# Kernel tuning notes

Hardware: AMD Instinct MI355X
Metric: run time of the kernel (lower is better)

The kernel has to match this reference:

```python
import math
import jax, jax.numpy as jnp
import numpy as np

LMAX = 6
F_ACT = 16   # f_out // 8, channels through SO3Activation
F_MID = 64   # f_out // 2
N_A, N_B, N_C = 16, 8, 16  # SO(3) Euler-angle grid (resolution=8 quadrature in beta)
SQRT2 = math.sqrt(2.0)     # normalize2mom factor for relu

# ---- Wigner-D machinery (numpy, setup-time constants; mirrors e3nn conventions) ----

def _su2_generators(j):
    m = np.arange(-j, j)
    raising = np.diag(-np.sqrt(j * (j + 1) - m * (m + 1)), k=-1).astype(complex)
    m = np.arange(-j + 1, j + 1)
    lowering = np.diag(np.sqrt(j * (j + 1) - m * (m - 1)), k=1).astype(complex)
    m = np.arange(-j, j + 1)
    return np.stack([0.5 * (raising + lowering), np.diag(1j * m), -0.5j * (raising - lowering)])

def _q_real(l):
    q = np.zeros((2 * l + 1, 2 * l + 1), dtype=complex)
    for m in range(-l, 0):
        q[l + m, l + abs(m)] = 2 ** -0.5
        q[l + m, l - abs(m)] = -1j * 2 ** -0.5
    q[l, l] = 1
    for m in range(1, l + 1):
        q[l + m, l + abs(m)] = (-1) ** m * 2 ** -0.5
        q[l + m, l - abs(m)] = 1j * (-1) ** m * 2 ** -0.5
    return (-1j) ** l * q

def _so3_generators(l):
    X = _su2_generators(l)
    Q = _q_real(l)
    return np.real(np.einsum('ij,njk,kl->nil', np.conj(Q.T), X, Q))

def _expm(A):
    w, V = np.linalg.eig(A.astype(complex))
    return np.real((V * np.exp(w)) @ np.linalg.inv(V))

def _wigner_prod_grid(lmax, a, b, c):
    # flat_wigner on a product Euler grid: D(a,b,g) = exp(a*Jy) exp(b*Jx) exp(g*Jy)
    blocks = []
    for l in range(lmax + 1):
        X = _so3_generators(l)
        Ea = np.stack([_expm(t * X[1]) for t in a])
        Eb = np.stack([_expm(t * X[0]) for t in b])
        Ec = np.stack([_expm(t * X[1]) for t in c])
        D = np.einsum('amn,bnp,cpq->abcmq', Ea, Eb, Ec)
        blocks.append((2 * l + 1) ** 0.5 * D.reshape(len(a) * len(b) * len(c), -1))
    return np.concatenate(blocks, -1)

def _flat_wigner_pts(lmax, a, b, c):
    blocks = []
    for l in range(lmax + 1):
        X = _so3_generators(l)
        D = np.stack([_expm(ai * X[1]) @ _expm(bi * X[0]) @ _expm(ci * X[1]) for ai, bi, ci in zip(a, b, c)])
        blocks.append((2 * l + 1) ** 0.5 * D.reshape(len(a), -1))
    return np.concatenate(blocks, -1)

def _c8_angles():
    # escnn rot2dOnR2(8) elements, transposed and embedded into 3x3 with z fixed
    th = 2 * np.pi * np.arange(8) / 8
    M = np.zeros((8, 3, 3))
    M[:, 0, 0] = np.cos(th); M[:, 0, 1] = np.sin(th)
    M[:, 1, 0] = -np.sin(th); M[:, 1, 1] = np.cos(th)
    M[:, 2, 2] = 1.0
    x = M @ np.array([0.0, 1.0, 0.0])
    b = np.arccos(np.clip(x[:, 1], -1, 1))
    a = np.arctan2(x[:, 0], x[:, 2])
    def my(t): c, s = np.cos(t), np.sin(t); return np.array([[c, 0, s], [0, 1, 0], [-s, 0, c]])
    def mx(t): c, s = np.cos(t), np.sin(t); return np.array([[1, 0, 0], [0, c, -s], [0, s, c]])
    g = np.array([np.arctan2(R[0, 2], R[0, 0]) for R in [(my(a[i]) @ mx(b[i])).T @ M[i] for i in range(8)]])
    return a, b, g

# ---- precomputed constants ----
_A = 2 * np.pi * np.arange(N_A) / N_A
_XB, _WB = np.polynomial.legendre.leggauss(N_B)
_B = np.arccos(_XB)
_C = 2 * np.pi * np.arange(N_C) / N_C
D_IN = jnp.asarray(_wigner_prod_grid(1, _A, _B, _C), jnp.float32)                 # (G, 10)
_QW = np.broadcast_to((_WB / 2.0)[None, :, None] / (N_A * N_C), (N_A, N_B, N_C)).reshape(-1)
D_OUTW = jnp.asarray(_wigner_prod_grid(LMAX, _A, _B, _C) * _QW[:, None], jnp.float32)  # (G, 455), quadrature folded in
C8W = jnp.asarray(_flat_wigner_pts(LMAX, *_c8_angles()), jnp.float32)             # (8, 455)


def setup_inputs() -> dict:
    key = jax.random.key(0)
    ks = jax.random.split(key, 16)
    inp = {
        'x': jax.random.normal(ks[0], (16, 32, 128, 455), jnp.float32),
        'trajectory': jax.random.normal(ks[1], (16, 32, 10), jnp.float32),
        'w1_l0': jax.random.normal(ks[2], (1, F_ACT, 1, 1), jnp.float32),
        'w1_l1': jax.random.normal(ks[3], (1, F_ACT, 3, 3), jnp.float32),
    }
    for l in range(LMAX + 1):
        d = 2 * l + 1
        inp[f'w2_l{l}'] = jax.random.normal(ks[4 + l], (F_ACT, F_MID, d, d), jnp.float32)
    return inp


def reference(x, trajectory, w1_l0, w1_l1, w2_l0, w2_l1, w2_l2, w2_l3, w2_l4, w2_l5, w2_l6):
    w2s = [w2_l0, w2_l1, w2_l2, w2_l3, w2_l4, w2_l5, w2_l6]
    b, t, _ = trajectory.shape
    # pack trajectory into irreps 1x0e + 3x1e: scalar is last input component
    ti = jnp.concatenate([trajectory[..., 9:10], trajectory[..., :9]], axis=-1)  # (b,t,10)
    # proj_1 (o3.Linear, f_in=1 -> f_out=16), per-l block mixing with 1/sqrt(f_in*mul_in)
    o0 = ti[:, :, None, 0:1] * w1_l0[0, :, 0, 0][None, None, :, None]            # (b,t,16,1)
    x1 = ti[..., 1:10].reshape(b, t, 3, 3)                                       # (mul=3, m=3)
    o1 = jnp.einsum('btum,guw->btgwm', x1, w1_l1[0]) * (3.0 ** -0.5)             # (b,t,16,3,3)
    feat = jnp.concatenate([o0, o1.reshape(b, t, F_ACT, 9)], axis=-1)            # (b,t,16,10)
    # SO3Activation: irreps -> SO(3) grid -> relu (2nd-moment normalized) -> irreps up to LMAX
    sig = jnp.einsum('btci,gi->btcg', feat, D_IN)                                # (b,t,16,G)
    sig = jax.nn.relu(sig) * SQRT2
    feat = jnp.einsum('btcg,gi->btci', sig, D_OUTW)                              # (b,t,16,455)
    # proj_2 (o3.Linear on so3_irreps(6), f 16->64), block-diagonal per l
    outs = []
    off = 0
    for l in range(LMAX + 1):
        d = 2 * l + 1
        blk = feat[..., off:off + d * d].reshape(b, t, F_ACT, d, d)
        o = jnp.einsum('btfum,fguw->btgwm', blk, w2s[l]) * ((F_ACT * d) ** -0.5)
        outs.append(o.reshape(b, t, F_MID, d * d))
        off += d * d
    traj_out = jnp.concatenate(outs, axis=-1)                                    # (b,t,64,455)
    # Wigner-D projection onto C8 group elements
    traj_c8 = jnp.einsum('btcj,ij->btci', traj_out, C8W)                         # (b,t,64,8)
    x_c8 = jnp.einsum('bhcj,ij->bhci', x, C8W)                                   # (b,h,128,8)
    return x_c8, traj_c8
```

## Files before the change

### kernel.cpp

```cpp
#include <hip/hip_runtime.h>
#include <hip/hip_bf16.h>
#include <math.h>


typedef __attribute__((ext_vector_type(8))) short bf16x8;
typedef __attribute__((ext_vector_type(4))) float f32x4;
typedef __attribute__((ext_vector_type(16))) float f32x16;

__device__ const int c_offs[8] = {0, 1, 10, 35, 84, 165, 286, 455};

struct SetupArgs {
  double angA[16];
  double angB[8];
  double c8a[8], c8b[8], c8g[8];
};
struct QWArgs { double wb[8]; };
struct W2Ptrs { const void* p[7]; };

__device__ __forceinline__ float bf2f(unsigned short u) {
  union { unsigned int i; float f; } v; v.i = ((unsigned int)u) << 16; return v.f;
}
__device__ __forceinline__ unsigned short f2bf(float f) {
  union { float f; unsigned int i; } v; v.f = f;
  unsigned int r = v.i + 0x7fffu + ((v.i >> 16) & 1u);
  return (unsigned short)(r >> 16);
}
__device__ __forceinline__ float in_val(const void* p, size_t i, int isf) {
  return isf ? ((const float*)p)[i] : bf2f(((const unsigned short*)p)[i]);
}
__device__ __forceinline__ void gl_lds16(const void* g, void* lds) {
  __builtin_amdgcn_global_load_lds(
      (const __attribute__((address_space(1))) unsigned int*)g,
      (__attribute__((address_space(3))) unsigned int*)lds, 16, 0, 0);
}

__global__ __launch_bounds__(192) void k_exps(SetupArgs args, double* exps,
                                              const void* x, int* flag) {
  __shared__ double Qr[169], Qi[169], Bm[169], R[169];
  __shared__ double coefA[13], coefB[13], rowsum[13];
  __shared__ double snorm;
  __shared__ int cnt;
  int tid = threadIdx.x;

  if (blockIdx.x == 336) {
    if (tid == 0) cnt = 0;
    __syncthreads();
    if (tid < 64) {
      float v = ((const float*)x)[tid];
      float a = fabsf(v);
      int ok = (v == v) && (a > 9.0949470e-13f) && (a < 1.0995116e12f);
      atomicAdd(&cnt, ok);
    }
    __syncthreads();
    if (tid == 0) *flag = (cnt >= 32) ? 1 : 0;
    return;
  }

  int l = blockIdx.x / 48, item = blockIdx.x % 48;
  int e = tid;
  bool val = (e < 169);
  int r = e / 13, c = e % 13;

  if (val) { Qr[e] = 0.0; Qi[e] = 0.0; }
  __syncthreads();
  if (tid == 0) {
    const double is2 = 0.70710678118654752440;
    for (int m = -l; m <= l; m++) {
      int rr = l + m;
      if (m < 0) {
        Qr[rr * 13 + (l - m)] = is2;
        Qi[rr * 13 + (l + m)] = -is2;
      } else if (m == 0) {
        Qr[l * 13 + l] = 1.0;
      } else {
        double s = (m & 1) ? -1.0 : 1.0;
        Qr[rr * 13 + (l + m)] = s * is2;
        Qi[rr * 13 + (l - m)] = s * is2;
      }
    }
  }
  double jj = (double)l;
  if (tid < 13) {
    double m1 = (double)(tid - 1 - l);
    coefA[tid] = -0.5 * sqrt(fmax(jj * (jj + 1.0) - m1 * (m1 + 1.0), 0.0));
    double m2 = (double)(tid + 1 - l);
    coefB[tid] = 0.5 * sqrt(fmax(jj * (jj + 1.0) - m2 * (m2 - 1.0), 0.0));
  }
  __syncthreads();
  {
    int lm = l & 3;
    double pr = (lm == 0) ? 1.0 : (lm == 2 ? -1.0 : 0.0);
    double pi = (lm == 1) ? -1.0 : (lm == 3 ? 1.0 : 0.0);
    if (val) {
      double qr = Qr[e], qi = Qi[e];
      Qr[e] = qr * pr - qi * pi;
      Qi[e] = qr * pi + qi * pr;
    }
  }
  __syncthreads();

  double t; int axis;
  if (item < 16)      { t = args.angA[item];      axis = 1; }
  else if (item < 24) { t = args.angB[item - 16]; axis = 0; }
  else if (item < 32) { t = args.c8a[item - 24];  axis = 1; }
  else if (item < 40) { t = args.c8b[item - 32];  axis = 0; }
  else                { t = args.c8g[item - 40];  axis = 1; }

  if (val) {
    double accr = 0.0;
    if (axis == 1) {
#pragma unroll
      for (int p = 0; p < 13; p++) {
        double mp = (double)(p - l);
        double ar = Qr[p * 13 + r], ai = -Qi[p * 13 + r];
        double br = Qr[p * 13 + c], bi = Qi[p * 13 + c];
        accr += -mp * (ar * bi + ai * br);
      }
    } else {
#pragma unroll
      for (int p = 0; p < 13; p++) {
        double xr = 0.0, xi = 0.0;
        if (p > 0) {
          double v = coefA[p];
          xr += v * Qr[(p - 1) * 13 + c]; xi += v * Qi[(p - 1) * 13 + c];
        }
        if (p < 12) {
          double v = coefB[p];
          xr += v * Qr[(p + 1) * 13 + c]; xi += v * Qi[(p + 1) * 13 + c];
        }
        double ar = Qr[p * 13 + r], ai = -Qi[p * 13 + r];
        accr += ar * xr - ai * xi;
      }
    }
    Bm[e] = t * accr;
  }
  __syncthreads();
  if (tid < 13) {
    double s = 0.0;
#pragma unroll
    for (int cc = 0; cc < 13; cc++) s += fabs(Bm[tid * 13 + cc]);
    rowsum[tid] = s;
  }
  __syncthreads();
  if (tid == 0) {
    double mx = 0.0;
#pragma unroll
    for (int rr = 0; rr < 13; rr++) mx = fmax(mx, rowsum[rr]);
    int s = 0;
    while (mx > 0.5 && s < 48) { mx *= 0.5; s++; }
    snorm = (double)s;
  }
  __syncthreads();
  int sq = (int)snorm;
  double sc = 1.0;
  for (int i = 0; i < sq; i++) sc *= 0.5;
  if (val) {
    double b = Bm[e] * sc;
    Bm[e] = b;
    R[e] = b / 16.0 + ((r == c) ? 1.0 : 0.0);
  }
  __syncthreads();
  for (int k = 15; k >= 1; k--) {
    double acc = 0.0;
    if (val) {
#pragma unroll
      for (int p = 0; p < 13; p++) acc += Bm[r * 13 + p] * R[p * 13 + c];
    }
    __syncthreads();
    if (val) R[e] = acc / (double)k + ((r == c) ? 1.0 : 0.0);
    __syncthreads();
  }
  for (int i = 0; i < sq; i++) {
    double acc = 0.0;
    if (val) {
#pragma unroll
      for (int p = 0; p < 13; p++) acc += R[r * 13 + p] * R[p * 13 + c];
    }
    __syncthreads();
    if (val) R[e] = acc;
    __syncthreads();
  }
  double* out = exps + (size_t)blockIdx.x * 169;
  if (val) out[e] = R[e];
}

__global__ __launch_bounds__(192) void k_assemble(const double* exps, QWArgs qw,
                                                  unsigned short* dwt, float* dint,
                                                  float* c8w,
                                                  const void* traj, const void* w1l0,
                                                  const void* w1l1, float* feat,
                                                  const int* flag) {
  __shared__ double Ea[169], Eb[169], Ec[169], T1[169];
  int tid = threadIdx.x;
  int bx = blockIdx.x;

  if (bx >= 952) {
    int isf = __builtin_amdgcn_readfirstlane(flag[0]);
    int idx = (bx - 952) * 192 + tid;
    if (idx >= 512 * 160) return;
    int bt = idx / 160, rem = idx % 160;
    int c = rem / 10, i = rem % 10;
    float v;
    if (i == 0) {
      v = in_val(traj, bt * 10 + 9, isf) * in_val(w1l0, c, isf);
    } else {
      int ii = i - 1, w = ii / 3, m = ii % 3;
      float acc = 0.0f;
      for (int u = 0; u < 3; u++)
        acc += in_val(traj, bt * 10 + 3 * u + m, isf) *
               in_val(w1l1, c * 9 + u * 3 + w, isf);
      v = acc * 0.57735026918962576f;
    }
    feat[idx] = v;
    return;
  }

  int e = tid;
  bool valp = (e < 169);
  int r = e / 13, c = e % 13;

  if (bx >= 896) {
    int idx = bx - 896;
    int l = idx / 8, ci = idx % 8;
    int d = 2 * l + 1;
    const double* pa = exps + (size_t)(l * 48 + 24 + ci) * 169;
    const double* pb = exps + (size_t)(l * 48 + 32 + ci) * 169;
    const double* pc = exps + (size_t)(l * 48 + 40 + ci) * 169;
    if (valp) { Ea[e] = pa[e]; Eb[e] = pb[e]; Ec[e] = pc[e]; }
    __syncthreads();
    if (valp) {
      double acc = 0.0;
#pragma unroll
      for (int p = 0; p < 13; p++) acc += Ea[r * 13 + p] * Eb[p * 13 + c];
      T1[e] = acc;
    }
    __syncthreads();
    double scale = sqrt((double)(2 * l + 1));
    if (valp) {
      double acc = 0.0;
#pragma unroll
      for (int p = 0; p < 13; p++) acc += T1[r * 13 + p] * Ec[p * 13 + c];
      if (r < d && c < d)
        c8w[ci * 512 + c_offs[l] + r * d + c] = (float)(scale * acc);
    }
    if (l == 0) {
      for (int jz = 455 + tid; jz < 512; jz += 192)
        c8w[ci * 512 + jz] = 0.0f;
    }
    return;
  }

  int l = bx >> 7, rem = bx & 127;
  int a = rem >> 3, b = rem & 7;
  int d = 2 * l + 1;
  const double* pa = exps + (size_t)(l * 48 + a) * 169;
  const double* pb = exps + (size_t)(l * 48 + 16 + b) * 169;
  if (valp) { Ea[e] = pa[e]; Eb[e] = pb[e]; }
  __syncthreads();
  if (valp) {
    double acc = 0.0;
#pragma unroll
    for (int p = 0; p < 13; p++) acc += Ea[r * 13 + p] * Eb[p * 13 + c];
    T1[e] = acc;
  }
  double scale = sqrt((double)(2 * l + 1));
  double qwv = qw.wb[b] * (1.0 / 512.0);
  bool inblk = valp && (r < d) && (c < d);
  int j = inblk ? (c_offs[l] + r * d + c) : 0;
  int g0 = a * 128 + b * 16;
  const double* ctab = exps + (size_t)(l * 48) * 169;
  unsigned int ow[8];
  float dv[16];
#pragma unroll
  for (int cc = 0; cc < 16; cc++) {
    __syncthreads();
    if (valp) Ec[e] = ctab[(size_t)cc * 169 + e];
    __syncthreads();
    double acc = 0.0;
    if (valp) {
#pragma unroll
      for (int p = 0; p < 13; p++) acc += T1[r * 13 + p] * Ec[p * 13 + c];
    }
    unsigned int hv = (unsigned int)f2bf((float)(scale * acc * qwv));
    if ((cc & 1) == 0) ow[cc >> 1] = hv;
    else               ow[cc >> 1] |= hv << 16;
    dv[cc] = (float)(scale * acc);
  }
  if (inblk) {
    unsigned short* wp = &dwt[(size_t)j * 2048 + g0];
    *(uint4*)&wp[0] = make_uint4(ow[0], ow[1], ow[2], ow[3]);
    *(uint4*)&wp[8] = make_uint4(ow[4], ow[5], ow[6], ow[7]);
    if (l == 1) {
      float* dp = &dint[(size_t)(1 + r * 3 + c) * 2048 + g0];
      *(float4*)&dp[0]  = make_float4(dv[0],  dv[1],  dv[2],  dv[3]);
      *(float4*)&dp[4]  = make_float4(dv[4],  dv[5],  dv[6],  dv[7]);
      *(float4*)&dp[8]  = make_float4(dv[8],  dv[9],  dv[10], dv[11]);
      *(float4*)&dp[12] = make_float4(dv[12], dv[13], dv[14], dv[15]);
    }
    if (l == 0) {
      float* dp = &dint[g0];
      *(float4*)&dp[0]  = make_float4(dv[0],  dv[1],  dv[2],  dv[3]);
      *(float4*)&dp[4]  = make_float4(dv[4],  dv[5],  dv[6],  dv[7]);
      *(float4*)&dp[8]  = make_float4(dv[8],  dv[9],  dv[10], dv[11]);
      *(float4*)&dp[12] = make_float4(dv[12], dv[13], dv[14], dv[15]);
    }
  }
  if (l == 0 && tid < 57) {
    unsigned short* zp = &dwt[(size_t)(455 + tid) * 2048 + g0];
    *(uint4*)&zp[0] = make_uint4(0, 0, 0, 0);
    *(uint4*)&zp[8] = make_uint4(0, 0, 0, 0);
  }
}

__global__ __launch_bounds__(256) void k_post(const float* feat, const float* dint,
                                              unsigned short* sig, W2Ptrs w2,
                                              const float* c8w, unsigned short* et,
                                              const int* flag) {
  int bx = blockIdx.x;
  if (bx < 4096) {
    int bi = bx >> 3;
    int g = ((bx & 7) << 8) + threadIdx.x;
    float din[10];
#pragma unroll
    for (int i = 0; i < 10; i++) din[i] = dint[(size_t)i * 2048 + g];
    const float* fr = feat + bi * 160;
    for (int cc = 0; cc < 16; cc++) {
      float acc = 0.0f;
#pragma unroll
      for (int i = 0; i < 10; i++) acc += fr[cc * 10 + i] * din[i];
      acc = fmaxf(acc, 0.0f) * 1.41421356237309505f;
      sig[(size_t)(bi * 16 + cc) * 2048 + g] = f2bf(acc);
    }
    return;
  }
  int isf = __builtin_amdgcn_readfirstlane(flag[0]);
  int base = ((bx - 4096) * 256 + threadIdx.x) * 4;
  int n = base >> 13;
  int rest = base & 8191;
  int f = rest >> 9, jj0 = rest & 511;
  int g = n >> 3, i = n & 7;
  unsigned short ov[4];
#pragma unroll
  for (int s = 0; s < 4; s++) {
    int jj = jj0 + s;
    if (jj >= 455) { ov[s] = 0; continue; }
    int l    = (jj >= 1) + (jj >= 10) + (jj >= 35) + (jj >= 84) +
               (jj >= 165) + (jj >= 286);
    int offs = jj >= 286 ? 286 : jj >= 165 ? 165 : jj >= 84 ? 84 :
               jj >= 35 ? 35 : jj >= 10 ? 10 : jj >= 1 ? 1 : 0;
    int mg   = jj >= 286 ? 20165 : jj >= 165 ? 23832 : jj >= 84 ? 29128 :
               jj >= 35 ? 37450 : jj >= 10 ? 52429 : jj >= 1 ? 87382 : 262144;
    int d = 2 * l + 1;
    int rloc = jj - offs;
    int u = (rloc * mg) >> 18;
    int m = rloc - u * d;
    const void* wp = w2.p[0];
    wp = (l >= 1) ? w2.p[1] : wp;
    wp = (l >= 2) ? w2.p[2] : wp;
    wp = (l >= 3) ? w2.p[3] : wp;
    wp = (l >= 4) ? w2.p[4] : wp;
    wp = (l >= 5) ? w2.p[5] : wp;
    wp = (l >= 6) ? w2.p[6] : wp;
    float acc = 0.0f;
    for (int w = 0; w < d; w++) {
      float wv = in_val(wp, ((size_t)(f * 64 + g) * d + u) * d + w, isf);
      acc += wv * c8w[i * 512 + offs + w * d + m];
    }
    acc *= rsqrtf((float)(16 * d));
    ov[s] = f2bf(acc);
  }
  *(ushort4*)&et[(size_t)n * 8192 + f * 512 + jj0] =
      make_ushort4(ov[0], ov[1], ov[2], ov[3]);
}

__global__ __launch_bounds__(256) void k_gemm2(const unsigned short* A,
                                               const unsigned short* B,
                                               unsigned short* C) {
  __shared__ __align__(16) unsigned short As[3][128 * 64];
  __shared__ __align__(16) unsigned short Bs[3][64 * 64];
  int tid = threadIdx.x;
  int lane = tid & 63, wid = tid >> 6;
  int xcd = blockIdx.x & 7, bi = blockIdx.x >> 3;
  int mt = xcd * 8 + (bi >> 3), nt = bi & 7;
  int m0 = mt * 128, n0 = nt * 64;
  int wm = wid >> 1, wn = wid & 1;
  f32x16 acc[2];
#pragma unroll
  for (int t = 0; t < 2; t++)
#pragma unroll
    for (int r = 0; r < 16; r++) acc[t][r] = 0.0f;

  int r0 = tid >> 3;
  int kcl = (tid & 7) ^ (r0 & 7);
  const unsigned short* Abase = A + (size_t)m0 * 2048;
  const unsigned short* Bbase = B + (size_t)n0 * 2048;
  int mrow = (lane & 31);
  int xr = lane & 7;
  int khalf = lane >> 5;

  auto STAGE = [&](int buf, int kt) {
    int k0 = kt * 64;
#pragma unroll
    for (int i = 0; i < 4; i++)
      gl_lds16(Abase + (size_t)(i * 32 + r0) * 2048 + k0 + kcl * 8,
               &As[buf][i * 2048 + wid * 512]);
#pragma unroll
    for (int i = 0; i < 2; i++)
      gl_lds16(Bbase + (size_t)(i * 32 + r0) * 2048 + k0 + kcl * 8,
               &Bs[buf][i * 2048 + wid * 512]);
  };

  STAGE(0, 0);
  STAGE(1, 1);
  int cb = 0;
  for (int kt = 0; kt < 32; kt++) {
    if (kt < 31) asm volatile("s_waitcnt vmcnt(6)" ::: "memory");
    else         asm volatile("s_waitcnt vmcnt(0)" ::: "memory");
    __builtin_amdgcn_s_barrier();
    __builtin_amdgcn_sched_barrier(0);
    const unsigned short* Ab = As[cb];
    const unsigned short* Bb = Bs[cb];
#pragma unroll
    for (int q = 0; q < 4; q++) {
      int qc = q * 2 + khalf;
      bf16x8 bv = *(const bf16x8*)&Bb[(wn * 32 + mrow) * 64 + (qc ^ xr) * 8];
#pragma unroll
      for (int t = 0; t < 2; t++) {
        bf16x8 av = *(const bf16x8*)&Ab[(wm * 64 + t * 32 + mrow) * 64 + (qc ^ xr) * 8];
        acc[t] = __builtin_amdgcn_mfma_f32_32x32x16_bf16(av, bv, acc[t], 0, 0, 0);
      }
    }
    if (kt < 30) STAGE(cb == 0 ? 2 : cb - 1, kt + 2);
    cb = (cb == 2) ? 0 : cb + 1;
  }
  int col = n0 + wn * 32 + (lane & 31);
#pragma unroll
  for (int t = 0; t < 2; t++)
#pragma unroll
    for (int r = 0; r < 16; r++) {
      int row = m0 + wm * 64 + t * 32 + (r & 3) + 8 * (r >> 2) + 4 * (lane >> 5);
      C[(size_t)row * 512 + col] = f2bf(acc[t][r]);
    }
}

__global__ __launch_bounds__(256) void k_gemm3(const unsigned short* A,
                                               const unsigned short* B, float* Cp) {
  __shared__ __align__(16) unsigned short As[3][64 * 32];
  __shared__ __align__(16) unsigned short Bs[3][64 * 32];
  int tid = threadIdx.x, lane = tid & 63, wid = tid >> 6;
  int kc = blockIdx.x >> 6, mt = (blockIdx.x >> 3) & 7, nt = blockIdx.x & 7;
  int m0 = mt * 64, n0 = nt * 64;
  int wm = wid >> 1, wn = wid & 1;
  f32x4 acc[2][2];
#pragma unroll
  for (int a = 0; a < 2; a++)
#pragma unroll
    for (int b = 0; b < 2; b++) acc[a][b] = (f32x4){0.f, 0.f, 0.f, 0.f};
  int ar = tid >> 2, ak = (tid & 3) * 8;
  const unsigned short* Abase = A + (size_t)m0 * 8192 + kc * 1024;
  const unsigned short* Bbase = B + (size_t)n0 * 8192 + kc * 1024;
  int row = lane & 15, kq = (lane >> 4) * 8;

  auto STAGE = [&](int buf, int kt) {
    int k0 = kt * 32;
    gl_lds16(Abase + (size_t)ar * 8192 + k0 + ak, &As[buf][wid * 512]);
    gl_lds16(Bbase + (size_t)ar * 8192 + k0 + ak, &Bs[buf][wid * 512]);
  };

  STAGE(0, 0);
  STAGE(1, 1);
  int cb = 0;
  for (int kt = 0; kt < 32; kt++) {
    if (kt < 31) asm volatile("s_waitcnt vmcnt(2)" ::: "memory");
    else         asm volatile("s_waitcnt vmcnt(0)" ::: "memory");
    __builtin_amdgcn_s_barrier();
    __builtin_amdgcn_sched_barrier(0);
    bf16x8 af[2], bfr[2];
#pragma unroll
    for (int im = 0; im < 2; im++)
      af[im] = *(const bf16x8*)&As[cb][(wm * 32 + im * 16 + row) * 32 + kq];
#pragma unroll
    for (int in = 0; in < 2; in++)
      bfr[in] = *(const bf16x8*)&Bs[cb][(wn * 32 + in * 16 + row) * 32 + kq];
#pragma unroll
    for (int im = 0; im < 2; im++)
#pragma unroll
      for (int in = 0; in < 2; in++)
        acc[im][in] = __builtin_amdgcn_mfma_f32_16x16x32_bf16(af[im], bfr[in],
                                                              acc[im][in], 0, 0, 0);
    if (kt < 30) STAGE(cb == 0 ? 2 : cb - 1, kt + 2);
    cb = (cb == 2) ? 0 : cb + 1;
  }
  int col = lane & 15, rq = (lane >> 4) * 4;
  float* out = Cp + (size_t)kc * 262144;
#pragma unroll
  for (int im = 0; im < 2; im++)
#pragma unroll
    for (int in = 0; in < 2; in++)
#pragma unroll
      for (int r = 0; r < 4; r++) {
        int rr = m0 + wm * 32 + im * 16 + rq + r;
        int cc = n0 + wn * 32 + in * 16 + col;
        out[(size_t)rr * 512 + cc] = acc[im][in][r];
      }
}

__global__ __launch_bounds__(256) void k_xc8r(const void* x, const float* c8w,
                                              const float* Cp, void* dout,
                                              const int* flag) {
  int tid = threadIdx.x, lane = tid & 63, wid = tid >> 6;
  int isf = __builtin_amdgcn_readfirstlane(flag[0]);

  if (blockIdx.x >= 2048) {
    int idx = (blockIdx.x - 2048) * 256 + tid;
    const float4* c = (const float4*)Cp;
    float s0 = 0.f, s1 = 0.f, s2 = 0.f, s3 = 0.f;
#pragma unroll
    for (int p = 0; p < 8; p++) {
      float4 v = c[idx + p * 65536];
      s0 += v.x; s1 += v.y; s2 += v.z; s3 += v.w;
    }
    size_t base = 524288 + (size_t)idx * 4;
    if (isf) {
      float4 o; o.x = s0; o.y = s1; o.z = s2; o.w = s3;
      *(float4*)((float*)dout + base) = o;
    } else {
      unsigned int p0 = (unsigned int)f2bf(s0) | ((unsigned int)f2bf(s1) << 16);
      unsigned int p1 = (unsigned int)f2bf(s2) | ((unsigned int)f2bf(s3) << 16);
      uint2 pk; pk.x = p0; pk.y = p1;
      *(uint2*)((unsigned short*)dout + base) = pk;
    }
    return;
  }

  int gw = blockIdx.x * 4 + wid;
  float cw[8][8];
#pragma unroll
  for (int t = 0; t < 8; t++)
#pragma unroll
    for (int i = 0; i < 8; i++)
      cw[t][i] = c8w[i * 512 + t * 64 + lane];
  const float* xf = (const float*)x;
  const unsigned short* xh = (const unsigned short*)x;
  for (int r = gw * 8; r < gw * 8 + 8; r++) {
    float acc[8];
#pragma unroll
    for (int i = 0; i < 8; i++) acc[i] = 0.0f;
    if (isf) {
      const float* xr = xf + (size_t)r * 455;
#pragma unroll
      for (int t = 0; t < 8; t++) {
        int j = t * 64 + lane;
        float xv = (j < 455) ? xr[j] : 0.0f;
#pragma unroll
        for (int i = 0; i < 8; i++) acc[i] += xv * cw[t][i];
      }
    } else {
      const unsigned short* xr = xh + (size_t)r * 455;
#pragma unroll
      for (int t = 0; t < 8; t++) {
        int j = t * 64 + lane;
        float xv = (j < 455) ? bf2f(xr[j]) : 0.0f;
#pragma unroll
        for (int i = 0; i < 8; i++) acc[i] += xv * cw[t][i];
      }
    }
#pragma unroll
    for (int off = 1; off <= 4; off <<= 1)
#pragma unroll
      for (int i = 0; i < 8; i++) acc[i] += __shfl_xor(acc[i], off);
    int lg = lane & 7;
    float v = acc[0];
    v = (lg == 1) ? acc[1] : v;
    v = (lg == 2) ? acc[2] : v;
    v = (lg == 3) ? acc[3] : v;
    v = (lg == 4) ? acc[4] : v;
    v = (lg == 5) ? acc[5] : v;
    v = (lg == 6) ? acc[6] : v;
    v = (lg == 7) ? acc[7] : v;
    v += __shfl_xor(v, 8);
    v += __shfl_xor(v, 16);
    v += __shfl_xor(v, 32);
    if (lane < 8) {
      if (isf) ((float*)dout)[(size_t)r * 8 + lane] = v;
      else     ((unsigned short*)dout)[(size_t)r * 8 + lane] = f2bf(v);
    }
  }
}

extern "C" void kernel_launch(void* const* d_in, const int* in_sizes, int n_in,
                              void* d_out, int out_size, void* d_ws, size_t ws_size,
                              hipStream_t stream) {
  const void* x    = d_in[0];
  const void* traj = d_in[1];
  const void* w1l0 = d_in[2];
  const void* w1l1 = d_in[3];
  W2Ptrs w2;
  for (int l = 0; l < 7; l++) w2.p[l] = d_in[4 + l];

  char* ws = (char*)d_ws;
  double* exps          = (double*)(ws + 0);
  float* dint           = (float*)(ws + 458752);
  float* c8w            = (float*)(ws + 540672);
  unsigned short* dwt   = (unsigned short*)(ws + 573440);
  float* feat           = (float*)(ws + 2670592);
  unsigned short* sig   = (unsigned short*)(ws + 2998272);
  unsigned short* f2    = (unsigned short*)(ws + 36552704);
  unsigned short* et    = (unsigned short*)(ws + 44941312);
  float* cp             = (float*)(ws + 53329920);
  int* flag             = (int*)(ws + 61718528);

  SetupArgs sa; QWArgs qa;
  for (int i = 0; i < 16; i++) sa.angA[i] = 2.0 * M_PI * (double)i / 16.0;
  static const double XB[8] = {
    -0.9602898564975363, -0.7966664774136267, -0.5255324099163290,
    -0.1834346424956498,  0.1834346424956498,  0.5255324099163290,
     0.7966664774136267,  0.9602898564975363};
  static const double WBv[8] = {
     0.1012285362903763, 0.2223810344533745, 0.3137066458778873,
     0.3626837833783620, 0.3626837833783620, 0.3137066458778873,
     0.2223810344533745, 0.1012285362903763};
  for (int i = 0; i < 8; i++) { sa.angB[i] = acos(XB[i]); qa.wb[i] = WBv[i]; }
  for (int i = 0; i < 8; i++) {
    double th = 2.0 * M_PI * (double)i / 8.0;
    double Mm[3][3] = {{cos(th), sin(th), 0.0},
                       {-sin(th), cos(th), 0.0},
                       {0.0, 0.0, 1.0}};
    double x0 = Mm[0][1], x1 = Mm[1][1], x2 = Mm[2][1];
    double bb = acos(fmax(-1.0, fmin(1.0, x1)));
    double aa = atan2(x0, x2);
    double ca_ = cos(aa), sa_ = sin(aa), cb_ = cos(bb), sb_ = sin(bb);
    double MY[3][3] = {{ca_, 0, sa_}, {0, 1, 0}, {-sa_, 0, ca_}};
    double MX[3][3] = {{1, 0, 0}, {0, cb_, -sb_}, {0, sb_, cb_}};
    double P1[3][3], Rr[3][3];
    for (int r = 0; r < 3; r++)
      for (int c = 0; c < 3; c++) {
        double s = 0.0;
        for (int k = 0; k < 3; k++) s += MY[r][k] * MX[k][c];
        P1[r][c] = s;
      }
    for (int r = 0; r < 3; r++)
      for (int c = 0; c < 3; c++) {
        double s = 0.0;
        for (int k = 0; k < 3; k++) s += P1[k][r] * Mm[k][c];
        Rr[r][c] = s;
      }
    double gg = atan2(Rr[0][2], Rr[0][0]);
    sa.c8a[i] = aa; sa.c8b[i] = bb; sa.c8g[i] = gg;
  }

  k_exps<<<337, 192, 0, stream>>>(sa, exps, x, flag);
  k_assemble<<<1379, 192, 0, stream>>>(exps, qa, dwt, dint, c8w,
                                       traj, w1l0, w1l1, feat, flag);
  k_post<<<8192, 256, 0, stream>>>(feat, dint, sig, w2, c8w, et, flag);
  k_gemm2<<<512, 256, 0, stream>>>(sig, dwt, f2);
  k_gemm3<<<512, 256, 0, stream>>>(f2, et, cp);
  k_xc8r<<<2304, 256, 0, stream>>>(x, c8w, cp, d_out, flag);
}
```

Before: 327.8 us.

## Restructure k_post: LDS-tiled per-l et builder, separate zero pad, paired sig writes

The et construction (w2 block times C8 Wigner projection) now runs one templated body per degree l. Each block stages a slice of w2 and the C8 coefficients in shared memory and computes full rows in registers, replacing the per-element scalar loop that re-read global memory for every output. The padding columns are zeroed by dedicated blocks, and the sig relu-projection part now handles two grid points per thread with packed bf16 stores. This cuts the grid from 8192 to 3456 blocks, but l=6 blocks do more work than the others, so the load may be unbalanced.

Result: faster. 271.6 us (-17.2%).

```diff
diff --git a/kernel.cpp b/kernel.cpp
--- a/kernel.cpp
+++ b/kernel.cpp
@@ -312,48 +312,61 @@
   }
 }
 
+template <int D>
+__device__ __forceinline__ void ebuild_body(int f, int g0, const void* wp,
+                                            const float* c8w, unsigned short* et,
+                                            int isf, int offs,
+                                            float* w2s, float* c8p) {
+  const int d2 = D * D;
+  int tid = threadIdx.x;
+  size_t gbase = ((size_t)f * 64 + g0) * d2;
+  for (int e = tid; e < 8 * d2; e += 256) {
+    int r = e / D, w = e - r * D;
+    w2s[r * 16 + w] = in_val(wp, gbase + e, isf);
+  }
+  for (int e = tid; e < 8 * d2; e += 256) {
+    int i = e / d2, k = e - i * d2;
+    int w = k / D, m = k - w * D;
+    c8p[(i * D + w) * 16 + m] = c8w[i * 512 + offs + k];
+  }
+  __syncthreads();
+  const float rs = rsqrtf((float)(16 * D));
+  for (int R = tid; R < 64 * D; R += 256) {
+    int gi = R / D, u = R - gi * D;
+    int g = gi >> 3, i = gi & 7;
+    float wrow[D];
+#pragma unroll
+    for (int w = 0; w < D; w++) wrow[w] = w2s[(g * D + u) * 16 + w];
+    float accv[D];
+#pragma unroll
+    for (int m = 0; m < D; m++) accv[m] = 0.0f;
+#pragma unroll
+    for (int w = 0; w < D; w++)
+#pragma unroll
+      for (int m = 0; m < D; m++)
+        accv[m] += wrow[w] * c8p[(i * D + w) * 16 + m];
+    unsigned short* orow =
+        &et[(size_t)((g0 + g) * 8 + i) * 8192 + f * 512 + offs + u * D];
+#pragma unroll
+    for (int m = 0; m < D; m++) orow[m] = f2bf(accv[m] * rs);
+  }
+}
+
 __global__ __launch_bounds__(256) void k_post(const float* feat, const float* dint,
                                               unsigned short* sig, W2Ptrs w2,
                                               const float* c8w, unsigned short* et,
                                               const int* flag) {
+  __shared__ float w2s[1664], c8p[1664];
   int bx = blockIdx.x;
-  if (bx < 4096) {
-    int bi = bx >> 3;
-    int g = ((bx & 7) << 8) + threadIdx.x;
-    float din[10];
-#pragma unroll
-    for (int i = 0; i < 10; i++) din[i] = dint[(size_t)i * 2048 + g];
-    const float* fr = feat + bi * 160;
-    for (int cc = 0; cc < 16; cc++) {
-      float acc = 0.0f;
-#pragma unroll
-      for (int i = 0; i < 10; i++) acc += fr[cc * 10 + i] * din[i];
-      acc = fmaxf(acc, 0.0f) * 1.41421356237309505f;
-      sig[(size_t)(bi * 16 + cc) * 2048 + g] = f2bf(acc);
-    }
-    return;
-  }
-  int isf = __builtin_amdgcn_readfirstlane(flag[0]);
-  int base = ((bx - 4096) * 256 + threadIdx.x) * 4;
-  int n = base >> 13;
-  int rest = base & 8191;
-  int f = rest >> 9, jj0 = rest & 511;
-  int g = n >> 3, i = n & 7;
-  unsigned short ov[4];
-#pragma unroll
-  for (int s = 0; s < 4; s++) {
-    int jj = jj0 + s;
-    if (jj >= 455) { ov[s] = 0; continue; }
-    int l    = (jj >= 1) + (jj >= 10) + (jj >= 35) + (jj >= 84) +
-               (jj >= 165) + (jj >= 286);
-    int offs = jj >= 286 ? 286 : jj >= 165 ? 165 : jj >= 84 ? 84 :
-               jj >= 35 ? 35 : jj >= 10 ? 10 : jj >= 1 ? 1 : 0;
-    int mg   = jj >= 286 ? 20165 : jj >= 165 ? 23832 : jj >= 84 ? 29128 :
-               jj >= 35 ? 37450 : jj >= 10 ? 52429 : jj >= 1 ? 87382 : 262144;
-    int d = 2 * l + 1;
-    int rloc = jj - offs;
-    int u = (rloc * mg) >> 18;
-    int m = rloc - u * d;
+  int tid = threadIdx.x;
+
+  if (bx < 896) {
+    int isf = __builtin_amdgcn_readfirstlane(flag[0]);
+    int li = bx >> 7;
+    int l = 6 - li;
+    int rem = bx & 127;
+    int f = rem >> 3, g0 = (rem & 7) * 8;
+    int offs = c_offs[l];
     const void* wp = w2.p[0];
     wp = (l >= 1) ? w2.p[1] : wp;
     wp = (l >= 2) ? w2.p[2] : wp;
@@ -361,16 +374,52 @@
     wp = (l >= 4) ? w2.p[4] : wp;
     wp = (l >= 5) ? w2.p[5] : wp;
     wp = (l >= 6) ? w2.p[6] : wp;
-    float acc = 0.0f;
-    for (int w = 0; w < d; w++) {
-      float wv = in_val(wp, ((size_t)(f * 64 + g) * d + u) * d + w, isf);
-      acc += wv * c8w[i * 512 + offs + w * d + m];
-    }
-    acc *= rsqrtf((float)(16 * d));
-    ov[s] = f2bf(acc);
-  }
-  *(ushort4*)&et[(size_t)n * 8192 + f * 512 + jj0] =
-      make_ushort4(ov[0], ov[1], ov[2], ov[3]);
+    switch (l) {
+      case 6: ebuild_body<13>(f, g0, wp, c8w, et, isf, offs, w2s, c8p); break;
+      case 5: ebuild_body<11>(f, g0, wp, c8w, et, isf, offs, w2s, c8p); break;
+      case 4: ebuild_body<9>(f, g0, wp, c8w, et, isf, offs, w2s, c8p); break;
+      case 3: ebuild_body<7>(f, g0, wp, c8w, et, isf, offs, w2s, c8p); break;
+      case 2: ebuild_body<5>(f, g0, wp, c8w, et, isf, offs, w2s, c8p); break;
+      case 1: ebuild_body<3>(f, g0, wp, c8w, et, isf, offs, w2s, c8p); break;
+      default: ebuild_body<1>(f, g0, wp, c8w, et, isf, offs, w2s, c8p); break;
+    }
+    return;
+  }
+
+  if (bx < 1408) {
+    int n = bx - 896;
+    int f = tid >> 4, k = tid & 15;
+#pragma unroll
+    for (int s = 0; s < 4; s++) {
+      int jj = 455 + k + s * 16;
+      if (jj < 512) et[(size_t)n * 8192 + f * 512 + jj] = 0;
+    }
+    return;
+  }
+
+  int bx2 = bx - 1408;
+  int bi = bx2 >> 2;
+  int g0 = ((bx2 & 3) << 9) + tid * 2;
+  float din0[10], din1[10];
+#pragma unroll
+  for (int i = 0; i < 10; i++) {
+    float2 dv = *(const float2*)&dint[(size_t)i * 2048 + g0];
+    din0[i] = dv.x; din1[i] = dv.y;
+  }
+  const float* fr = feat + bi * 160;
+  for (int cc = 0; cc < 16; cc++) {
+    float a0 = 0.0f, a1 = 0.0f;
+#pragma unroll
+    for (int i = 0; i < 10; i++) {
+      float fv = fr[cc * 10 + i];
+      a0 += fv * din0[i];
+      a1 += fv * din1[i];
+    }
+    a0 = fmaxf(a0, 0.0f) * 1.41421356237309505f;
+    a1 = fmaxf(a1, 0.0f) * 1.41421356237309505f;
+    unsigned int pk = (unsigned int)f2bf(a0) | ((unsigned int)f2bf(a1) << 16);
+    *(unsigned int*)&sig[(size_t)(bi * 16 + cc) * 2048 + g0] = pk;
+  }
 }
 
 __global__ __launch_bounds__(256) void k_gemm2(const unsigned short* A,
@@ -652,7 +701,7 @@
   k_exps<<<337, 192, 0, stream>>>(sa, exps, x, flag);
   k_assemble<<<1379, 192, 0, stream>>>(exps, qa, dwt, dint, c8w,
                                        traj, w1l0, w1l1, feat, flag);
-  k_post<<<8192, 256, 0, stream>>>(feat, dint, sig, w2, c8w, et, flag);
+  k_post<<<3456, 256, 0, stream>>>(feat, dint, sig, w2, c8w, et, flag);
   k_gemm2<<<512, 256, 0, stream>>>(sig, dwt, f2);
   k_gemm3<<<512, 256, 0, stream>>>(f2, et, cp);
   k_xc8r<<<2304, 256, 0, stream>>>(x, c8w, cp, d_out, flag);
```
